# Performance work log

Measured on AMD Instinct MI355X. Metric: run time of the kernel, lower is better.

The kernel has to match this reference:

```python
import jax, jax.numpy as jnp
import numpy as np

H = 128; L = 4; N_TOTAL = 2500; M = 4; K = 12
S = N_TOTAL * M          # 10000 subgraphs
F = S * K                # 120000 flat nodes
E_INTRA = 2 * F          # 240000 intra-subgraph edges
E_INTER = 16 * N_TOTAL   # 40000 canonical edges
B = 50; VOCAB = 119; MAX_DIST = 32; BN_EPS = 1e-5


def _bn(x, g, b):
    # training-mode BatchNorm1d over rows (biased var, eps=1e-5)
    mu = x.mean(0)
    var = x.var(0)
    return (x - mu) * jax.lax.rsqrt(var + BN_EPS) * g + b


def _gine(x, ei, ea, W1, b1, W2, b2):
    # PyG GINEConv, eps=0: MLP(x + sum_{src->dst} relu(x[src] + e))
    msg = jax.nn.relu(x[ei[0]] + ea)                              # [E,H]
    agg = jax.ops.segment_sum(msg, ei[1], num_segments=x.shape[0])
    h = x + agg
    return jax.nn.relu(h @ W1 + b1) @ W2 + b2


def setup_inputs():
    key = jax.random.key(0)
    ks = list(jax.random.split(key, 32)); it = iter(ks)
    nk = lambda: next(it)
    rn = lambda shape, s=0.05: jax.random.normal(nk(), shape, dtype=jnp.float32) * s
    x_tok = jax.random.randint(nk(), (F,), 0, VOCAB)
    dist = jax.random.randint(nk(), (F,), 0, MAX_DIST + 1)
    node_ids = jax.random.randint(nk(), (F,), 0, N_TOTAL)
    node_ids = jnp.where(jax.random.uniform(nk(), (F,)) < 0.1, -1, node_ids)
    root_flat_idx = jnp.arange(S) * K
    node_ids = node_ids.at[root_flat_idx].set(jnp.arange(S) // M)  # root = canonical node
    valid = node_ids >= 0
    sub_batch = jnp.repeat(jnp.arange(S), K)
    src = jax.random.randint(nk(), (E_INTRA,), 0, F)
    dst = (src // K) * K + jax.random.randint(nk(), (E_INTRA,), 0, K)  # stay inside subgraph
    intra_ei = jnp.stack([src, dst])
    edge_index = jax.random.randint(nk(), (2, E_INTER), 0, N_TOTAL)
    batch_ids = jnp.arange(N_TOTAL) // (N_TOTAL // B)
    lp = -jax.random.uniform(nk(), (S,)) * 3.0                    # log-probs <= 0
    z = lambda *shape: jnp.zeros(shape, jnp.float32)
    o = lambda *shape: jnp.ones(shape, jnp.float32)
    return dict(
        x_tok=x_tok, dist=dist, node_ids=node_ids, valid=valid,
        sub_batch=sub_batch, root_flat_idx=root_flat_idx,
        intra_ei=intra_ei, edge_index=edge_index, batch_ids=batch_ids,
        lp=lp, ea_flat=rn((E_INTRA, H)), edge_attr=rn((E_INTER, H)),
        atom_emb=rn((VOCAB, H)), dist_emb=rn((MAX_DIST + 1, H)),
        logp_w=rn((1, H)), logp_b=z(H),
        intra_W1=rn((L, H, H)), intra_b1=z(L, H),
        intra_W2=rn((L, H, H)), intra_b2=z(L, H),
        intra_bn_g=o(L, H), intra_bn_b=z(L, H),
        self_W=rn((L, H, H)), self_b=z(L, H),
        root_W=rn((L, H, H)), root_b=z(L, H),
        inter_W1=rn((L, H, H)), inter_b1=z(L, H),
        inter_W2=rn((L, H, H)), inter_b2=z(L, H),
        inter_bn_g=o(L, H), inter_bn_b=z(L, H),
        readout_bn_g=o(H), readout_bn_b=z(H),
        alpha_pool=o(1), alpha_inter=o(1),
    )


def reference(x_tok, dist, node_ids, valid, sub_batch, root_flat_idx, intra_ei,
              edge_index, batch_ids, lp, ea_flat, edge_attr, atom_emb, dist_emb,
              logp_w, logp_b, intra_W1, intra_b1, intra_W2, intra_b2,
              intra_bn_g, intra_bn_b, self_W, self_b, root_W, root_b,
              inter_W1, inter_b1, inter_W2, inter_b2, inter_bn_g, inter_bn_b,
              readout_bn_g, readout_bn_b, alpha_pool, alpha_inter):
    valid_f = valid.astype(jnp.float32)[:, None]                  # [F,1]
    is_root_f = jnp.zeros((F, 1), jnp.float32).at[root_flat_idx].set(1.0)
    clamped_ids = jnp.maximum(node_ids, 0)
    # input encoding: atom embedding + BFS-distance PE + log-prob PE
    logp_pe = jax.nn.relu(lp[sub_batch][:, None] * logp_w[0] + logp_b)
    h = (atom_emb[x_tok] + dist_emb[dist] + logp_pe) * valid_f
    # HT inter-root weights, normalized per canonical root id
    root_ids = node_ids[root_flat_idx]                            # [S]
    rv = root_ids >= 0
    rid = jnp.maximum(root_ids, 0)
    w_un = jnp.where(rv, jnp.exp(-alpha_inter[0] * lp), 0.0)
    w_sum = jax.ops.segment_sum(w_un, rid, num_segments=N_TOTAL)
    ht_w = jnp.where(rv, w_un / (w_sum[rid] + 1e-16), 0.0)        # [S]
    for l in range(L):
        h1 = _gine(h, intra_ei, ea_flat, intra_W1[l], intra_b1[l], intra_W2[l], intra_b2[l])
        h1 = _bn(h1, intra_bn_g[l], intra_bn_b[l]) * valid_f
        h_root_bcast = h[sub_batch * K]
        h_non_root = (h @ self_W[l] + self_b[l]) + (h_root_bcast @ root_W[l] + root_b[l])
        # HT-weighted scatter of root reps to canonical nodes
        h_roots = h[root_flat_idx]                                # [S,H]
        h_root_canon = jax.ops.segment_sum(h_roots * ht_w[:, None], rid, num_segments=N_TOTAL)
        h_inter = _gine(h_root_canon, edge_index, edge_attr, inter_W1[l], inter_b1[l], inter_W2[l], inter_b2[l])
        h_inter = _bn(h_inter, inter_bn_g[l], inter_bn_b[l])
        h_inter_bcast = h_inter[clamped_ids] * valid_f
        out = is_root_f * (h1 + h_inter_bcast) + (1.0 - is_root_f) * (h1 + h_non_root)
        h = jax.nn.relu(out) * valid_f                            # dropout p=0
    # HT softmax readout over the m subgraphs of each canonical node
    h_sub = jax.ops.segment_sum(h * valid_f, sub_batch, num_segments=S)
    h_sub_2d = h_sub.reshape(N_TOTAL, M, H)
    w = jax.nn.softmax(-alpha_pool[0] * lp.reshape(N_TOTAL, M), axis=1)
    node_emb = jnp.einsum('nm,nmh->nh', w, h_sub_2d)
    node_emb = _bn(node_emb, readout_bn_g, readout_bn_b)
    return jax.ops.segment_sum(node_emb, batch_ids, num_segments=B)  # [B,H]
```

## Files before the change

kernel.cpp:

```cpp
#include <hip/hip_runtime.h>
#include <math.h>

#define H 128
#define H4 (H/4)
#define KK 12
#define MSUB 4
#define FF 120000
#define SS 10000
#define NN 2500
#define NBATCH 50
#define NLAYER 4
#define EINTRA 240000
#define EINTER 40000
#define HH (H*H)
#define BN_EPS 1e-5f
#define CAP_I 32
#define CAP_E 96


__global__ void k_zero(float* __restrict__ p, int n){
  int i = blockIdx.x*256 + threadIdx.x;
  if (i < n) p[i] = 0.f;
}

__global__ void k_zeroi(int* __restrict__ p, int n){
  int i = blockIdx.x*256 + threadIdx.x;
  if (i < n) p[i] = 0;
}


__global__ void k_bucket(const int* __restrict__ dst, int E, int* __restrict__ cnt,
                         int* __restrict__ beid, int cap){
  int e = blockIdx.x*256 + threadIdx.x;
  if (e >= E) return;
  int d = dst[e];
  int p = atomicAdd(&cnt[d], 1);
  if (p < cap) beid[(size_t)d*cap + p] = e;
}


__global__ void k_encode(float* __restrict__ h, const int* __restrict__ xtok,
                         const int* __restrict__ dist, const int* __restrict__ nids,
                         const int* __restrict__ subb, const float* __restrict__ lp,
                         const float* __restrict__ aemb, const float* __restrict__ demb,
                         const float* __restrict__ lw, const float* __restrict__ lb){
  int idx = blockIdx.x*256 + threadIdx.x;
  if (idx >= FF*H4) return;
  int f = idx >> 5; int c = (idx & 31) << 2;
  float vf = (nids[f] >= 0) ? 1.f : 0.f;
  float l = lp[subb[f]];
  float4 a = *(const float4*)(aemb + (size_t)xtok[f]*H + c);
  float4 d = *(const float4*)(demb + (size_t)dist[f]*H + c);
  float4 w = *(const float4*)(lw + c);
  float4 b = *(const float4*)(lb + c);
  float4 o;
  o.x = (a.x + d.x + fmaxf(fmaf(l, w.x, b.x), 0.f)) * vf;
  o.y = (a.y + d.y + fmaxf(fmaf(l, w.y, b.y), 0.f)) * vf;
  o.z = (a.z + d.z + fmaxf(fmaf(l, w.z, b.z), 0.f)) * vf;
  o.w = (a.w + d.w + fmaxf(fmaf(l, w.w, b.w), 0.f)) * vf;
  *(float4*)(h + (size_t)f*H + c) = o;
}


__global__ void k_htw(const int* __restrict__ nids, const int* __restrict__ rfi,
                      const float* __restrict__ lp, const float* __restrict__ alpha,
                      float* __restrict__ htw){
  int n = blockIdx.x*256 + threadIdx.x;
  if (n >= NN) return;
  float a = alpha[0];
  float w[MSUB]; float sum = 0.f;
  #pragma unroll
  for (int m = 0; m < MSUB; ++m){
    int s = n*MSUB + m;
    int rid = nids[rfi[s]];
    float wm = (rid >= 0) ? expf(-a*lp[s]) : 0.f;
    w[m] = wm; sum += wm;
  }
  float inv = 1.f / (sum + 1e-16f);
  #pragma unroll
  for (int m = 0; m < MSUB; ++m) htw[n*MSUB + m] = w[m]*inv;
}


__global__ void k_gine_gather(float* __restrict__ outa, const float* __restrict__ x,
                              const float* __restrict__ ea, const int* __restrict__ cnt,
                              const int* __restrict__ beid, const int* __restrict__ src,
                              int rows, int cap){
  int idx = blockIdx.x*256 + threadIdx.x;
  if (idx >= rows*H4) return;
  int f = idx >> 5; int c = (idx & 31) << 2;
  float4 acc = *(const float4*)(x + (size_t)f*H + c);
  int n = cnt[f]; if (n > cap) n = cap;
  const int* bl = beid + (size_t)f*cap;
  for (int i = 0; i < n; ++i){
    int e = bl[i];
    int s = src[e];
    float4 xv = *(const float4*)(x + (size_t)s*H + c);
    float4 ev = *(const float4*)(ea + (size_t)e*H + c);
    acc.x += fmaxf(xv.x + ev.x, 0.f);
    acc.y += fmaxf(xv.y + ev.y, 0.f);
    acc.z += fmaxf(xv.z + ev.z, 0.f);
    acc.w += fmaxf(xv.w + ev.w, 0.f);
  }
  *(float4*)(outa + (size_t)f*H + c) = acc;
}


__global__ void k_canon(float* __restrict__ canon, const float* __restrict__ h,
                        const float* __restrict__ htw, const int* __restrict__ rfi){
  int idx = blockIdx.x*256 + threadIdx.x;
  if (idx >= NN*H4) return;
  int n = idx >> 5; int c = (idx & 31) << 2;
  float4 acc = make_float4(0.f,0.f,0.f,0.f);
  #pragma unroll
  for (int m = 0; m < MSUB; ++m){
    int s = n*MSUB + m;
    float w = htw[s];
    const float* p = h + (size_t)rfi[s]*H + c;
    acc.x += w*p[0]; acc.y += w*p[1]; acc.z += w*p[2]; acc.w += w*p[3];
  }
  *(float4*)(canon + (size_t)n*H + c) = acc;
}


__global__ __launch_bounds__(256) void k_matmul(const float* __restrict__ in, float* __restrict__ out,
    int rows, const float* __restrict__ W, const float* __restrict__ bias,
    int do_relu, const int* __restrict__ gather){
  __shared__ __align__(16) float w[H*64];
  __shared__ __align__(16) float xs[16][H+4];
  __shared__ float bsh[64];
  int tid = threadIdx.x;
  int cbase = blockIdx.y * 64;
  for (int i = tid; i < H*16; i += 256){
    int k = i >> 4, j4 = i & 15;
    ((float4*)w)[i] = *(const float4*)(W + (size_t)k*H + cbase + (j4<<2));
  }
  if (tid < 64) bsh[tid] = bias[cbase + tid];
  __syncthreads();
  int row = tid >> 4; int lane = tid & 15; int lc = lane << 2;
  int ngroups = (rows + 15) >> 4;
  for (int g = blockIdx.x; g < ngroups; g += gridDim.x){
    int r = (g << 4) + row;
    bool ok = r < rows;
    if (ok){
      int ir = gather ? gather[r] : r;
      const float* srcp = in + (size_t)ir*H + (lane<<3);
      *(float4*)&xs[row][lane<<3]     = *(const float4*)srcp;
      *(float4*)&xs[row][(lane<<3)+4] = *(const float4*)(srcp+4);
    }
    __syncthreads();
    if (ok){
      float4 acc = *(float4*)&bsh[lc];
      #pragma unroll
      for (int k4 = 0; k4 < 32; ++k4){
        float4 xv = *(float4*)&xs[row][k4<<2];
        float4 w0 = *(float4*)&w[((k4<<2)+0)*64 + lc];
        float4 w1 = *(float4*)&w[((k4<<2)+1)*64 + lc];
        float4 w2 = *(float4*)&w[((k4<<2)+2)*64 + lc];
        float4 w3 = *(float4*)&w[((k4<<2)+3)*64 + lc];
        acc.x = fmaf(xv.x,w0.x,acc.x); acc.y = fmaf(xv.x,w0.y,acc.y); acc.z = fmaf(xv.x,w0.z,acc.z); acc.w = fmaf(xv.x,w0.w,acc.w);
        acc.x = fmaf(xv.y,w1.x,acc.x); acc.y = fmaf(xv.y,w1.y,acc.y); acc.z = fmaf(xv.y,w1.z,acc.z); acc.w = fmaf(xv.y,w1.w,acc.w);
        acc.x = fmaf(xv.z,w2.x,acc.x); acc.y = fmaf(xv.z,w2.y,acc.y); acc.z = fmaf(xv.z,w2.z,acc.z); acc.w = fmaf(xv.z,w2.w,acc.w);
        acc.x = fmaf(xv.w,w3.x,acc.x); acc.y = fmaf(xv.w,w3.y,acc.y); acc.z = fmaf(xv.w,w3.z,acc.z); acc.w = fmaf(xv.w,w3.w,acc.w);
      }
      if (do_relu){
        acc.x=fmaxf(acc.x,0.f); acc.y=fmaxf(acc.y,0.f); acc.z=fmaxf(acc.z,0.f); acc.w=fmaxf(acc.w,0.f);
      }
      *(float4*)(out + (size_t)r*H + cbase + lc) = acc;
    }
    __syncthreads();
  }
}


__global__ void k_bnstats(const float* __restrict__ x, int rows, double* __restrict__ stats){
  int g = blockIdx.x*256 + threadIdx.x;
  int c = g & (H-1);
  int rstart = g >> 7;
  int rstride = (gridDim.x*256) >> 7;
  double s = 0.0, s2 = 0.0;
  for (int r = rstart; r < rows; r += rstride){
    float v = x[(size_t)r*H + c];
    s += v; s2 += (double)v*(double)v;
  }
  atomicAdd(&stats[c], s);
  atomicAdd(&stats[H+c], s2);
}

__global__ void k_bnfin(double* __restrict__ stats, int rows, float* __restrict__ muinv){
  int c = threadIdx.x;
  if (c < H){
    double mu = stats[c] / (double)rows;
    double var = stats[H+c] / (double)rows - mu*mu;
    muinv[c]   = (float)mu;
    muinv[H+c] = (float)(1.0 / sqrt(var + (double)BN_EPS));
    stats[c] = 0.0; stats[H+c] = 0.0;
  }
}

__global__ void k_bnapply(float* __restrict__ x, const float* __restrict__ muinv,
                          const float* __restrict__ g, const float* __restrict__ b, int rows){
  int idx = blockIdx.x*256 + threadIdx.x;
  if (idx >= rows*H4) return;
  int r = idx >> 5; int c = (idx & 31) << 2;
  float4 v  = *(const float4*)(x + (size_t)r*H + c);
  float4 mu = *(const float4*)(muinv + c);
  float4 iv = *(const float4*)(muinv + H + c);
  float4 gg = *(const float4*)(g + c);
  float4 bb = *(const float4*)(b + c);
  v.x = (v.x-mu.x)*iv.x*gg.x + bb.x;
  v.y = (v.y-mu.y)*iv.y*gg.y + bb.y;
  v.z = (v.z-mu.z)*iv.z*gg.z + bb.z;
  v.w = (v.w-mu.w)*iv.w*gg.w + bb.w;
  *(float4*)(x + (size_t)r*H + c) = v;
}


__global__ void k_combine(float* __restrict__ h, const float* __restrict__ h1raw,
                          const float* __restrict__ r1, const float* __restrict__ r2,
                          const float* __restrict__ hinter, const float* __restrict__ muinv,
                          const float* __restrict__ bg, const float* __restrict__ bb,
                          const int* __restrict__ nids){
  int idx = blockIdx.x*256 + threadIdx.x;
  if (idx >= FF*H4) return;
  int f = idx >> 5; int c = (idx & 31) << 2;
  int nid = nids[f];
  float vf = (nid >= 0) ? 1.f : 0.f;
  int cid = (nid < 0) ? 0 : nid;
  float4 x  = *(const float4*)(h1raw + (size_t)f*H + c);
  float4 mu = *(const float4*)(muinv + c);
  float4 iv = *(const float4*)(muinv + H + c);
  float4 g4 = *(const float4*)(bg + c);
  float4 b4 = *(const float4*)(bb + c);
  float4 h1;
  h1.x = ((x.x-mu.x)*iv.x*g4.x + b4.x) * vf;
  h1.y = ((x.y-mu.y)*iv.y*g4.y + b4.y) * vf;
  h1.z = ((x.z-mu.z)*iv.z*g4.z + b4.z) * vf;
  h1.w = ((x.w-mu.w)*iv.w*g4.w + b4.w) * vf;
  float4 o;
  if (f % KK == 0){
    float4 hi = *(const float4*)(hinter + (size_t)cid*H + c);
    o.x = h1.x + hi.x*vf; o.y = h1.y + hi.y*vf; o.z = h1.z + hi.z*vf; o.w = h1.w + hi.w*vf;
  } else {
    float4 a  = *(const float4*)(r1 + (size_t)f*H + c);
    float4 rr = *(const float4*)(r2 + (size_t)(f/KK)*H + c);
    o.x = h1.x + a.x + rr.x; o.y = h1.y + a.y + rr.y; o.z = h1.z + a.z + rr.z; o.w = h1.w + a.w + rr.w;
  }
  o.x = fmaxf(o.x,0.f)*vf; o.y = fmaxf(o.y,0.f)*vf; o.z = fmaxf(o.z,0.f)*vf; o.w = fmaxf(o.w,0.f)*vf;
  *(float4*)(h + (size_t)f*H + c) = o;
}


__global__ void k_hsub(float* __restrict__ hsub, const float* __restrict__ h){
  int idx = blockIdx.x*256 + threadIdx.x;
  if (idx >= SS*H4) return;
  int s = idx >> 5; int c = (idx & 31) << 2;
  float4 acc = make_float4(0.f,0.f,0.f,0.f);
  const float* base = h + (size_t)s*KK*H + c;
  #pragma unroll
  for (int k = 0; k < KK; ++k){
    float4 v = *(const float4*)(base + (size_t)k*H);
    acc.x += v.x; acc.y += v.y; acc.z += v.z; acc.w += v.w;
  }
  *(float4*)(hsub + (size_t)s*H + c) = acc;
}

__global__ void k_poolw(float* __restrict__ poolw, const float* __restrict__ lp,
                        const float* __restrict__ alpha){
  int n = blockIdx.x*256 + threadIdx.x;
  if (n >= NN) return;
  float a = alpha[0];
  float s0 = -a*lp[n*MSUB+0], s1 = -a*lp[n*MSUB+1], s2 = -a*lp[n*MSUB+2], s3 = -a*lp[n*MSUB+3];
  float m = fmaxf(fmaxf(s0,s1), fmaxf(s2,s3));
  float e0 = expf(s0-m), e1 = expf(s1-m), e2 = expf(s2-m), e3 = expf(s3-m);
  float sum = e0+e1+e2+e3;
  poolw[n*MSUB+0] = e0/sum; poolw[n*MSUB+1] = e1/sum;
  poolw[n*MSUB+2] = e2/sum; poolw[n*MSUB+3] = e3/sum;
}

__global__ void k_nodeemb(float* __restrict__ nemb, const float* __restrict__ hsub,
                          const float* __restrict__ poolw){
  int idx = blockIdx.x*256 + threadIdx.x;
  if (idx >= NN*H4) return;
  int n = idx >> 5; int c = (idx & 31) << 2;
  float w0 = poolw[n*MSUB+0], w1 = poolw[n*MSUB+1], w2 = poolw[n*MSUB+2], w3 = poolw[n*MSUB+3];
  const float* base = hsub + (size_t)n*MSUB*H + c;
  float4 v0 = *(const float4*)(base + 0*H);
  float4 v1 = *(const float4*)(base + 1*H);
  float4 v2 = *(const float4*)(base + 2*H);
  float4 v3 = *(const float4*)(base + 3*H);
  float4 o;
  o.x = w0*v0.x + w1*v1.x + w2*v2.x + w3*v3.x;
  o.y = w0*v0.y + w1*v1.y + w2*v2.y + w3*v3.y;
  o.z = w0*v0.z + w1*v1.z + w2*v2.z + w3*v3.z;
  o.w = w0*v0.w + w1*v1.w + w2*v2.w + w3*v3.w;
  *(float4*)(nemb + (size_t)n*H + c) = o;
}

__global__ void k_out(float* __restrict__ out, const float* __restrict__ nemb,
                      const float* __restrict__ muinv, const float* __restrict__ g,
                      const float* __restrict__ b){
  int idx = blockIdx.x*256 + threadIdx.x;
  if (idx >= NBATCH*H) return;
  int bi = idx >> 7; int c = idx & (H-1);
  float mu = muinv[c], iv = muinv[H+c], gg = g[c], bb = b[c];
  float acc = 0.f;
  const float* base = nemb + (size_t)bi*(NN/NBATCH)*H + c;
  for (int i = 0; i < NN/NBATCH; ++i)
    acc += (base[(size_t)i*H] - mu)*iv*gg + bb;
  out[idx] = acc;
}


extern "C" void kernel_launch(void* const* d_in, const int* in_sizes, int n_in,
                              void* d_out, int out_size, void* d_ws, size_t ws_size,
                              hipStream_t stream) {
  const int*   x_tok      = (const int*)  d_in[0];
  const int*   dist       = (const int*)  d_in[1];
  const int*   node_ids   = (const int*)  d_in[2];
  const int*   sub_batch  = (const int*)  d_in[4];
  const int*   rfi        = (const int*)  d_in[5];
  const int*   intra_ei   = (const int*)  d_in[6];
  const int*   edge_index = (const int*)  d_in[7];
  const float* lp         = (const float*)d_in[9];
  const float* ea_flat    = (const float*)d_in[10];
  const float* edge_attr  = (const float*)d_in[11];
  const float* atom_emb   = (const float*)d_in[12];
  const float* dist_emb   = (const float*)d_in[13];
  const float* logp_w     = (const float*)d_in[14];
  const float* logp_b     = (const float*)d_in[15];
  const float* intra_W1   = (const float*)d_in[16];
  const float* intra_b1   = (const float*)d_in[17];
  const float* intra_W2   = (const float*)d_in[18];
  const float* intra_b2   = (const float*)d_in[19];
  const float* intra_bn_g = (const float*)d_in[20];
  const float* intra_bn_b = (const float*)d_in[21];
  const float* self_W     = (const float*)d_in[22];
  const float* self_b     = (const float*)d_in[23];
  const float* root_W     = (const float*)d_in[24];
  const float* root_b     = (const float*)d_in[25];
  const float* inter_W1   = (const float*)d_in[26];
  const float* inter_b1   = (const float*)d_in[27];
  const float* inter_W2   = (const float*)d_in[28];
  const float* inter_b2   = (const float*)d_in[29];
  const float* inter_bn_g = (const float*)d_in[30];
  const float* inter_bn_b = (const float*)d_in[31];
  const float* ro_bn_g    = (const float*)d_in[32];
  const float* ro_bn_b    = (const float*)d_in[33];
  const float* alpha_pool = (const float*)d_in[34];
  const float* alpha_inter= (const float*)d_in[35];

  const int* isrc = intra_ei;
  const int* idst = intra_ei + EINTRA;
  const int* esrc = edge_index;
  const int* edst = edge_index + EINTER;

  float* out = (float*)d_out;

  char* ws = (char*)d_ws;
  size_t off = 0;
  auto nxt = [&](size_t bytes) -> void* {
    void* p = ws + off;
    off += (bytes + 255) & ~(size_t)255;
    return p;
  };
  float*  h      = (float*) nxt((size_t)FF*H*4);
  float*  hmid   = (float*) nxt((size_t)FF*H*4);
  float*  tbuf   = (float*) nxt((size_t)FF*H*4);
  float*  r2     = (float*) nxt((size_t)SS*H*4);
  float*  canon  = (float*) nxt((size_t)NN*H*4);
  float*  agg2   = (float*) nxt((size_t)NN*H*4);
  float*  hsub   = (float*) nxt((size_t)SS*H*4);
  float*  nemb   = (float*) nxt((size_t)NN*H*4);
  float*  htw    = (float*) nxt((size_t)SS*4);
  float*  poolw  = (float*) nxt((size_t)NN*MSUB*4);
  double* statsA = (double*)nxt((size_t)2*H*8);
  double* statsB = (double*)nxt((size_t)2*H*8);
  float*  muinvA = (float*) nxt((size_t)2*H*4);
  float*  muinvB = (float*) nxt((size_t)2*H*4);
  int*    icnt   = (int*)   nxt((size_t)FF*4);
  int*    ibeid  = (int*)   nxt((size_t)FF*CAP_I*4);
  int*    ecnt   = (int*)   nxt((size_t)NN*4);
  int*    ebeid  = (int*)   nxt((size_t)NN*CAP_E*4);
  (void)ws_size; (void)n_in; (void)in_sizes; (void)out_size; (void)sub_batch;

  const int G_FH4 = FF*H4/256;
  const int G_SH4 = SS*H4/256;
  const int G_NH4 = (NN*H4 + 255)/256;
  const int G_N   = (NN + 255)/256;

  k_zero<<<2, 256, 0, stream>>>((float*)statsA, 2*H*2);
  k_zero<<<2, 256, 0, stream>>>((float*)statsB, 2*H*2);
  k_zeroi<<<(FF+255)/256, 256, 0, stream>>>(icnt, FF);
  k_zeroi<<<G_N, 256, 0, stream>>>(ecnt, NN);

  k_bucket<<<(EINTRA+255)/256, 256, 0, stream>>>(idst, EINTRA, icnt, ibeid, CAP_I);
  k_bucket<<<(EINTER+255)/256, 256, 0, stream>>>(edst, EINTER, ecnt, ebeid, CAP_E);

  k_encode<<<G_FH4, 256, 0, stream>>>(h, x_tok, dist, node_ids, sub_batch, lp,
                                      atom_emb, dist_emb, logp_w, logp_b);
  k_htw<<<G_N, 256, 0, stream>>>(node_ids, rfi, lp, alpha_inter, htw);

  for (int l = 0; l < NLAYER; ++l){
    const float* W1 = intra_W1 + (size_t)l*HH; const float* b1 = intra_b1 + (size_t)l*H;
    const float* W2 = intra_W2 + (size_t)l*HH; const float* b2 = intra_b2 + (size_t)l*H;

    k_gine_gather<<<G_FH4, 256, 0, stream>>>(hmid, h, ea_flat, icnt, ibeid, isrc, FF, CAP_I);
    k_matmul<<<dim3(768,2), 256, 0, stream>>>(hmid, tbuf, FF, W1, b1, 1, nullptr);
    k_matmul<<<dim3(768,2), 256, 0, stream>>>(tbuf, hmid, FF, W2, b2, 0, nullptr);
    k_bnstats<<<512, 256, 0, stream>>>(hmid, FF, statsA);
    k_bnfin<<<1, 128, 0, stream>>>(statsA, FF, muinvA);

    k_canon<<<G_NH4, 256, 0, stream>>>(canon, h, htw, rfi);
    k_matmul<<<dim3(625,2), 256, 0, stream>>>(h, r2, SS, root_W + (size_t)l*HH,
                                              root_b + (size_t)l*H, 0, rfi);

    k_gine_gather<<<G_NH4, 256, 0, stream>>>(agg2, canon, edge_attr, ecnt, ebeid, esrc, NN, CAP_E);
    k_matmul<<<dim3(157,2), 256, 0, stream>>>(agg2, tbuf, NN, inter_W1 + (size_t)l*HH,
                                              inter_b1 + (size_t)l*H, 1, nullptr);
    k_matmul<<<dim3(157,2), 256, 0, stream>>>(tbuf, agg2, NN, inter_W2 + (size_t)l*HH,
                                              inter_b2 + (size_t)l*H, 0, nullptr);
    k_bnstats<<<128, 256, 0, stream>>>(agg2, NN, statsB);
    k_bnfin<<<1, 128, 0, stream>>>(statsB, NN, muinvB);
    k_bnapply<<<G_NH4, 256, 0, stream>>>(agg2, muinvB, inter_bn_g + (size_t)l*H,
                                         inter_bn_b + (size_t)l*H, NN);

    k_matmul<<<dim3(768,2), 256, 0, stream>>>(h, tbuf, FF, self_W + (size_t)l*HH,
                                              self_b + (size_t)l*H, 0, nullptr);
    k_combine<<<G_FH4, 256, 0, stream>>>(h, hmid, tbuf, r2, agg2, muinvA,
                                         intra_bn_g + (size_t)l*H,
                                         intra_bn_b + (size_t)l*H, node_ids);
  }

  k_hsub<<<G_SH4, 256, 0, stream>>>(hsub, h);
  k_poolw<<<G_N, 256, 0, stream>>>(poolw, lp, alpha_pool);
  k_nodeemb<<<G_NH4, 256, 0, stream>>>(nemb, hsub, poolw);
  k_bnstats<<<128, 256, 0, stream>>>(nemb, NN, statsB);
  k_bnfin<<<1, 128, 0, stream>>>(statsB, NN, muinvB);
  k_out<<<(NBATCH*H+255)/256, 256, 0, stream>>>(out, nemb, muinvB, ro_bn_g, ro_bn_b);
}
```

Baseline: 2.180 ms.

## Replace FP32 SIMT matmul with split-bf16 MFMA matmul kernel

Replaces the scalar-FMA 128x128 matmul with an MFMA kernel that splits each fp32 operand into high and low bf16 parts and issues three bf16 MFMAs per tile, keeping close to fp32 accuracy. Weights are pre-split into fragment layout in shared memory, each block handles 64 rows across all 128 columns, and grids are resized to match. This targets the compute-bound FP32 FMA cost of the large per-layer GEMMs. The trade-off is extra conversion work, dropping the lo*lo term (a small precision loss), and uncoalesced scalar output stores.

Measured after the change: 2.005 ms. 1.09x faster.

```diff
diff --git a/kernel.cpp b/kernel.cpp
--- a/kernel.cpp
+++ b/kernel.cpp
@@ -17,6 +17,15 @@
 #define CAP_I 32
 #define CAP_E 96
 
+typedef short short8 __attribute__((ext_vector_type(8)));
+typedef float floatx4 __attribute__((ext_vector_type(4)));
+
+__device__ __forceinline__ unsigned short f2bf_rne(float x){
+  unsigned u = __float_as_uint(x);
+  unsigned r = u + 0x7FFFu + ((u >> 16) & 1u);
+  return (unsigned short)(r >> 16);
+}
+
 
 __global__ void k_zero(float* __restrict__ p, int n){
   int i = blockIdx.x*256 + threadIdx.x;
@@ -123,52 +132,84 @@
 }
 
 
-__global__ __launch_bounds__(256) void k_matmul(const float* __restrict__ in, float* __restrict__ out,
-    int rows, const float* __restrict__ W, const float* __restrict__ bias,
-    int do_relu, const int* __restrict__ gather){
-  __shared__ __align__(16) float w[H*64];
-  __shared__ __align__(16) float xs[16][H+4];
-  __shared__ float bsh[64];
+__global__ __launch_bounds__(256, 2) void k_mm_mfma(
+    const float* __restrict__ in, float* __restrict__ out, int rows,
+    const float* __restrict__ W, const float* __restrict__ bias,
+    int do_relu, const int* __restrict__ gather)
+{
+  __shared__ __align__(16) short wfrag[2][4][8][64][8];
   int tid = threadIdx.x;
-  int cbase = blockIdx.y * 64;
-  for (int i = tid; i < H*16; i += 256){
-    int k = i >> 4, j4 = i & 15;
-    ((float4*)w)[i] = *(const float4*)(W + (size_t)k*H + cbase + (j4<<2));
-  }
-  if (tid < 64) bsh[tid] = bias[cbase + tid];
+  int w = tid >> 6, l = tid & 63;
+  int quad = l >> 4, n15 = l & 15;
+
+  #pragma unroll
+  for (int i = 0; i < 8; ++i){
+    int c = w + (i << 2);
+    int ks = c >> 3, nt = c & 7;
+    #pragma unroll
+    for (int j = 0; j < 8; ++j){
+      int k = ks*32 + quad*8 + j;
+      int n = nt*16 + n15;
+      float v = W[(size_t)k*H + n];
+      unsigned short hb = f2bf_rne(v);
+      float hf = __uint_as_float((unsigned)hb << 16);
+      unsigned short lb = f2bf_rne(v - hf);
+      wfrag[0][ks][nt][l][j] = (short)hb;
+      wfrag[1][ks][nt][l][j] = (short)lb;
+    }
+  }
   __syncthreads();
-  int row = tid >> 4; int lane = tid & 15; int lc = lane << 2;
-  int ngroups = (rows + 15) >> 4;
+
+  int ngroups = (rows + 63) >> 6;
   for (int g = blockIdx.x; g < ngroups; g += gridDim.x){
-    int r = (g << 4) + row;
-    bool ok = r < rows;
-    if (ok){
-      int ir = gather ? gather[r] : r;
-      const float* srcp = in + (size_t)ir*H + (lane<<3);
-      *(float4*)&xs[row][lane<<3]     = *(const float4*)srcp;
-      *(float4*)&xs[row][(lane<<3)+4] = *(const float4*)(srcp+4);
+    int rload = g*64 + w*16 + n15;
+    bool okload = rload < rows;
+    int ir = okload ? (gather ? gather[rload] : rload) : 0;
+    const float* ap = in + (size_t)ir*H + quad*8;
+
+    short8 ah[4], al[4];
+    #pragma unroll
+    for (int ks = 0; ks < 4; ++ks){
+      float4 a0 = okload ? *(const float4*)(ap + ks*32 + 0) : make_float4(0.f,0.f,0.f,0.f);
+      float4 a1 = okload ? *(const float4*)(ap + ks*32 + 4) : make_float4(0.f,0.f,0.f,0.f);
+      float av[8] = {a0.x,a0.y,a0.z,a0.w,a1.x,a1.y,a1.z,a1.w};
+      #pragma unroll
+      for (int j = 0; j < 8; ++j){
+        unsigned short hb = f2bf_rne(av[j]);
+        float hf = __uint_as_float((unsigned)hb << 16);
+        ah[ks][j] = (short)hb;
+        al[ks][j] = (short)f2bf_rne(av[j] - hf);
+      }
     }
-    __syncthreads();
-    if (ok){
-      float4 acc = *(float4*)&bsh[lc];
+
+    floatx4 acc[8] = {};
+    #pragma unroll
+    for (int ks = 0; ks < 4; ++ks){
       #pragma unroll
-      for (int k4 = 0; k4 < 32; ++k4){
-        float4 xv = *(float4*)&xs[row][k4<<2];
-        float4 w0 = *(float4*)&w[((k4<<2)+0)*64 + lc];
-        float4 w1 = *(float4*)&w[((k4<<2)+1)*64 + lc];
-        float4 w2 = *(float4*)&w[((k4<<2)+2)*64 + lc];
-        float4 w3 = *(float4*)&w[((k4<<2)+3)*64 + lc];
-        acc.x = fmaf(xv.x,w0.x,acc.x); acc.y = fmaf(xv.x,w0.y,acc.y); acc.z = fmaf(xv.x,w0.z,acc.z); acc.w = fmaf(xv.x,w0.w,acc.w);
-        acc.x = fmaf(xv.y,w1.x,acc.x); acc.y = fmaf(xv.y,w1.y,acc.y); acc.z = fmaf(xv.y,w1.z,acc.z); acc.w = fmaf(xv.y,w1.w,acc.w);
-        acc.x = fmaf(xv.z,w2.x,acc.x); acc.y = fmaf(xv.z,w2.y,acc.y); acc.z = fmaf(xv.z,w2.z,acc.z); acc.w = fmaf(xv.z,w2.w,acc.w);
-        acc.x = fmaf(xv.w,w3.x,acc.x); acc.y = fmaf(xv.w,w3.y,acc.y); acc.z = fmaf(xv.w,w3.z,acc.z); acc.w = fmaf(xv.w,w3.w,acc.w);
+      for (int nt = 0; nt < 8; ++nt){
+        short8 bh = *(const short8*)&wfrag[0][ks][nt][l][0];
+        short8 bl = *(const short8*)&wfrag[1][ks][nt][l][0];
+        acc[nt] = __builtin_amdgcn_mfma_f32_16x16x32_bf16(ah[ks], bh, acc[nt], 0, 0, 0);
+        acc[nt] = __builtin_amdgcn_mfma_f32_16x16x32_bf16(al[ks], bh, acc[nt], 0, 0, 0);
+        acc[nt] = __builtin_amdgcn_mfma_f32_16x16x32_bf16(ah[ks], bl, acc[nt], 0, 0, 0);
       }
-      if (do_relu){
-        acc.x=fmaxf(acc.x,0.f); acc.y=fmaxf(acc.y,0.f); acc.z=fmaxf(acc.z,0.f); acc.w=fmaxf(acc.w,0.f);
+    }
+
+    int rbase = g*64 + w*16 + quad*4;
+    #pragma unroll
+    for (int nt = 0; nt < 8; ++nt){
+      int col = nt*16 + n15;
+      float bv = bias[col];
+      #pragma unroll
+      for (int reg = 0; reg < 4; ++reg){
+        int r = rbase + reg;
+        if (r < rows){
+          float v = acc[nt][reg] + bv;
+          if (do_relu) v = fmaxf(v, 0.f);
+          out[(size_t)r*H + col] = v;
+        }
       }
-      *(float4*)(out + (size_t)r*H + cbase + lc) = acc;
     }
-    __syncthreads();
   }
 }
 
@@ -388,6 +429,9 @@
   const int G_SH4 = SS*H4/256;
   const int G_NH4 = (NN*H4 + 255)/256;
   const int G_N   = (NN + 255)/256;
+  const int G_MM_F = 512;
+  const int G_MM_S = (SS + 63)/64;
+  const int G_MM_N = (NN + 63)/64;
 
   k_zero<<<2, 256, 0, stream>>>((float*)statsA, 2*H*2);
   k_zero<<<2, 256, 0, stream>>>((float*)statsB, 2*H*2);
@@ -406,27 +450,27 @@
     const float* W2 = intra_W2 + (size_t)l*HH; const float* b2 = intra_b2 + (size_t)l*H;
 
     k_gine_gather<<<G_FH4, 256, 0, stream>>>(hmid, h, ea_flat, icnt, ibeid, isrc, FF, CAP_I);
-    k_matmul<<<dim3(768,2), 256, 0, stream>>>(hmid, tbuf, FF, W1, b1, 1, nullptr);
-    k_matmul<<<dim3(768,2), 256, 0, stream>>>(tbuf, hmid, FF, W2, b2, 0, nullptr);
+    k_mm_mfma<<<G_MM_F, 256, 0, stream>>>(hmid, tbuf, FF, W1, b1, 1, nullptr);
+    k_mm_mfma<<<G_MM_F, 256, 0, stream>>>(tbuf, hmid, FF, W2, b2, 0, nullptr);
     k_bnstats<<<512, 256, 0, stream>>>(hmid, FF, statsA);
     k_bnfin<<<1, 128, 0, stream>>>(statsA, FF, muinvA);
 
     k_canon<<<G_NH4, 256, 0, stream>>>(canon, h, htw, rfi);
-    k_matmul<<<dim3(625,2), 256, 0, stream>>>(h, r2, SS, root_W + (size_t)l*HH,
-                                              root_b + (size_t)l*H, 0, rfi);
+    k_mm_mfma<<<G_MM_S, 256, 0, stream>>>(h, r2, SS, root_W + (size_t)l*HH,
+                                          root_b + (size_t)l*H, 0, rfi);
 
     k_gine_gather<<<G_NH4, 256, 0, stream>>>(agg2, canon, edge_attr, ecnt, ebeid, esrc, NN, CAP_E);
-    k_matmul<<<dim3(157,2), 256, 0, stream>>>(agg2, tbuf, NN, inter_W1 + (size_t)l*HH,
-                                              inter_b1 + (size_t)l*H, 1, nullptr);
-    k_matmul<<<dim3(157,2), 256, 0, stream>>>(tbuf, agg2, NN, inter_W2 + (size_t)l*HH,
-                                              inter_b2 + (size_t)l*H, 0, nullptr);
+    k_mm_mfma<<<G_MM_N, 256, 0, stream>>>(agg2, tbuf, NN, inter_W1 + (size_t)l*HH,
+                                          inter_b1 + (size_t)l*H, 1, nullptr);
+    k_mm_mfma<<<G_MM_N, 256, 0, stream>>>(tbuf, agg2, NN, inter_W2 + (size_t)l*HH,
+                                          inter_b2 + (size_t)l*H, 0, nullptr);
     k_bnstats<<<128, 256, 0, stream>>>(agg2, NN, statsB);
     k_bnfin<<<1, 128, 0, stream>>>(statsB, NN, muinvB);
     k_bnapply<<<G_NH4, 256, 0, stream>>>(agg2, muinvB, inter_bn_g + (size_t)l*H,
                                          inter_bn_b + (size_t)l*H, NN);
 
-    k_matmul<<<dim3(768,2), 256, 0, stream>>>(h, tbuf, FF, self_W + (size_t)l*HH,
-                                              self_b + (size_t)l*H, 0, nullptr);
+    k_mm_mfma<<<G_MM_F, 256, 0, stream>>>(h, tbuf, FF, self_W + (size_t)l*HH,
+                                          self_b + (size_t)l*H, 0, nullptr);
     k_combine<<<G_FH4, 256, 0, stream>>>(h, hmid, tbuf, r2, agg2, muinvA,
                                          intra_bn_g + (size_t)l*H,
                                          intra_bn_b + (size_t)l*H, node_ids);
```
